# Kernel tuning notes

Measured on AMD Instinct MI355X. Metric: run time of the kernel, lower is better.

Reference implementation:

```python
import jax, jax.numpy as jnp
import numpy as np

N = 100000
E = 1600000
D = 128      # input_dim == hidden_dim
C = 40       # output_dim
L = 3        # num_layers
EPS = 1e-12  # F.normalize eps


def setup_inputs() -> dict:
    key = jax.random.key(0)
    ks = jax.random.split(key, 8)
    x = jax.random.normal(ks[0], (N, D), dtype=jnp.float32)
    edge_index = jax.random.randint(ks[1], (2, E), 0, N, dtype=jnp.int64)
    s = 1.0 / np.sqrt(D)
    # SAGEConv: lin_l (neighbor path, with bias), lin_r (root path, no bias)
    Wl = jax.random.uniform(ks[2], (L, D, D), jnp.float32, -s, s)
    bl = jax.random.uniform(ks[3], (L, D), jnp.float32, -s, s)
    Wr = jax.random.uniform(ks[4], (L, D, D), jnp.float32, -s, s)
    Wlin = jax.random.uniform(ks[5], (C, D), jnp.float32, -s, s)
    blin = jax.random.uniform(ks[6], (C,), jnp.float32, -s, s)
    return {"x": x, "edge_index": edge_index, "Wl": Wl, "bl": bl,
            "Wr": Wr, "Wlin": Wlin, "blin": blin}


def reference(x, edge_index, Wl, bl, Wr, Wlin, blin):
    src, dst = edge_index[0], edge_index[1]
    # in-degree counts for mean aggregation (computed once, reused per layer)
    cnt = jax.ops.segment_sum(jnp.ones((E,), jnp.float32), dst, num_segments=N)
    inv_cnt = (1.0 / jnp.maximum(cnt, 1.0))[:, None]  # [N,1]
    z = x
    for i in range(L):
        msg = z[src]  # gather [E, D]
        agg = jax.ops.segment_sum(msg, dst, num_segments=N) * inv_cnt  # mean [N, D]
        out = agg @ Wl[i].T + bl[i] + z @ Wr[i].T
        # SAGEConv normalize=True: L2 normalize per node
        nrm = jnp.linalg.norm(out, axis=-1, keepdims=True)
        out = out / jnp.maximum(nrm, EPS)
        z = jax.nn.relu(out)  # dropout p=0 -> identity
    return z @ Wlin.T + blin  # [N, C]
```

## Files before the change

kernel.cpp:

```cpp
#include <hip/hip_runtime.h>


typedef __bf16 bf16x8 __attribute__((ext_vector_type(8)));
typedef float  f32x4  __attribute__((ext_vector_type(4)));

#define MFMA16(a, b, c) __builtin_amdgcn_mfma_f32_16x16x32_bf16((a), (b), (c), 0, 0, 0)

__device__ __forceinline__ unsigned rne_bf16(float f) {
  unsigned u = __float_as_uint(f);
  unsigned r = u + 0x7FFFu + ((u >> 16) & 1u);
  return r >> 16;
}

__device__ __forceinline__ float bf_lo(unsigned u) { return __uint_as_float(u << 16); }
__device__ __forceinline__ float bf_hi(unsigned u) { return __uint_as_float(u & 0xFFFF0000u); }


__global__ void gcur_init_k(int* __restrict__ gcur, int cap) {
  gcur[threadIdx.x] = threadIdx.x * cap;
}

__global__ __launch_bounds__(256) void bucketA_k(
    const int* __restrict__ src, const int* __restrict__ dst,
    int* __restrict__ gcur, unsigned* __restrict__ coarse, int E, int nc) {
  __shared__ int hist[128];
  __shared__ int sd[128];
  __shared__ int lpos[128];
  __shared__ int gbase[128];
  __shared__ unsigned stage[2048];
  __shared__ unsigned char sbuck[2048];

  const int tid = threadIdx.x;
  const int e0 = blockIdx.x * 2048;

  if (tid < 128) hist[tid] = 0;
  __syncthreads();

  int bv[8], pk[8];
#pragma unroll
  for (int j = 0; j < 8; ++j) {
    int e = e0 + j * 256 + tid;
    bv[j] = -1;
    if (e < E) {
      int s = src[e], d = dst[e];
      bv[j] = d >> 10;
      pk[j] = s | ((d & 1023) << 17);
      atomicAdd(&hist[bv[j]], 1);
    }
  }
  __syncthreads();

  if (tid < 128) sd[tid] = hist[tid];
  __syncthreads();
  for (int off = 1; off < 128; off <<= 1) {
    int t = 0;
    if (tid < 128 && tid >= off) t = sd[tid - off];
    __syncthreads();
    if (tid < 128) sd[tid] += t;
    __syncthreads();
  }
  if (tid < 128) {
    int excl = sd[tid] - hist[tid];
    lpos[tid] = excl;
    gbase[tid] = (tid < nc && hist[tid] > 0) ? atomicAdd(&gcur[tid], hist[tid]) : 0;
  }
  __syncthreads();

#pragma unroll
  for (int j = 0; j < 8; ++j) {
    if (bv[j] >= 0) {
      int slot = atomicAdd(&lpos[bv[j]], 1);
      stage[slot] = (unsigned)pk[j];
      sbuck[slot] = (unsigned char)bv[j];
    }
  }
  __syncthreads();

  const int total = sd[127];
  for (int i = tid; i < total; i += 256) {
    int b = sbuck[i];
    int excl = sd[b] - hist[b];
    coarse[gbase[b] + (i - excl)] = stage[i];
  }
}

__global__ void cscan_k(const int* __restrict__ gcur, int cap, int nc,
                        int* __restrict__ cbase) {
  __shared__ int sd[128];
  const int tid = threadIdx.x;
  int v = (tid < nc) ? (gcur[tid] - tid * cap) : 0;
  sd[tid] = v;
  __syncthreads();
  for (int off = 1; off < 128; off <<= 1) {
    int u = (tid >= off) ? sd[tid - off] : 0;
    __syncthreads();
    sd[tid] += u;
    __syncthreads();
  }
  cbase[tid] = sd[tid] - v;
  if (tid == 127) cbase[128] = sd[127];
}

__global__ __launch_bounds__(256) void bucketB_k(
    const int* __restrict__ cbase, const int* __restrict__ gcur,
    const unsigned* __restrict__ coarse, int cap,
    int* __restrict__ esrc, int* __restrict__ offsets,
    float* __restrict__ inv_cnt, int n) {
  __shared__ int hcnt[1024];
  __shared__ int cur[1024];
  __shared__ int sd[256];

  const int tid = threadIdx.x;
  const int b = blockIdx.x;
  const int base = b * 1024;
  const int nn = (n - base < 1024) ? (n - base) : 1024;
  const int wbeg = b * cap;
  const int wend = gcur[b];
  const int gdst = cbase[b];

  for (int j = tid; j < 1024; j += 256) hcnt[j] = 0;
  __syncthreads();
  for (int idx = wbeg + tid; idx < wend; idx += 256)
    atomicAdd(&hcnt[coarse[idx] >> 17], 1);
  __syncthreads();

  int b0 = hcnt[tid * 4], b1 = hcnt[tid * 4 + 1];
  int b2 = hcnt[tid * 4 + 2], b3 = hcnt[tid * 4 + 3];
  int tot = b0 + b1 + b2 + b3;
  sd[tid] = tot;
  __syncthreads();
  for (int off = 1; off < 256; off <<= 1) {
    int u = (tid >= off) ? sd[tid - off] : 0;
    __syncthreads();
    sd[tid] += u;
    __syncthreads();
  }
  int excl = gdst + sd[tid] - tot;
  cur[tid * 4]     = excl;
  cur[tid * 4 + 1] = excl + b0;
  cur[tid * 4 + 2] = excl + b0 + b1;
  cur[tid * 4 + 3] = excl + b0 + b1 + b2;
  __syncthreads();

  for (int j = tid; j < nn; j += 256) {
    offsets[base + j] = cur[j];
    int c = hcnt[j] > 1 ? hcnt[j] : 1;
    inv_cnt[base + j] = 1.0f / (float)c;
  }
  if (tid == 0 && base + nn >= n) offsets[n] = gdst + (wend - wbeg);
  __syncthreads();

  for (int idx = wbeg + tid; idx < wend; idx += 256) {
    unsigned p = coarse[idx];
    int pos = atomicAdd(&cur[p >> 17], 1);
    esrc[pos] = (int)(p & 0x1FFFFu);
  }
}

__global__ void to_bf16_k(const float4* __restrict__ in, uint2* __restrict__ out, int n4) {
  int i = blockIdx.x * 256 + threadIdx.x;
  if (i >= n4) return;
  float4 f = in[i];
  uint2 o;
  o.x = rne_bf16(f.x) | (rne_bf16(f.y) << 16);
  o.y = rne_bf16(f.z) | (rne_bf16(f.w) << 16);
  out[i] = o;
}

__global__ void wfrag_prep_k(const float* __restrict__ Wl, const float* __restrict__ Wr,
                             unsigned short* __restrict__ wfrag) {
  int id = blockIdx.x * 256 + threadIdx.x;
  if (id >= 3 * 2 * 8 * 8 * 64) return;
  int l = id & 63;
  int c = (id >> 6) & 7;
  int t = (id >> 9) & 7;
  int p = (id >> 12) & 1;
  int layer = id >> 13;
  int col = t * 16 + (l & 15);
  int kbase = c * 32 + (l >> 4) * 8;
  unsigned short* dst = wfrag + (size_t)layer * 65536 +
                        ((((size_t)p * 8 + t) * 8 + c) * 64 + l) * 8;
#pragma unroll
  for (int j = 0; j < 8; ++j) {
    int k = kbase + j;
    float w = (k < 128) ? Wl[layer * 16384 + col * 128 + k]
                        : Wr[layer * 16384 + col * 128 + (k - 128)];
    unsigned h = rne_bf16(w);
    unsigned o;
    if (p == 0) o = h;
    else o = rne_bf16(w - __uint_as_float(h << 16));
    dst[j] = (unsigned short)o;
  }
}

__global__ void wlin_frag_k(const float* __restrict__ Wlin, unsigned short* __restrict__ wlf) {
  int id = blockIdx.x * 256 + threadIdx.x;
  if (id >= 3 * 4 * 64) return;
  int l = id & 63;
  int c = (id >> 6) & 3;
  int t = id >> 8;
  int col = t * 16 + (l & 15);
  int kbase = c * 32 + (l >> 4) * 8;
  unsigned short* dst = wlf + (size_t)id * 8;
#pragma unroll
  for (int j = 0; j < 8; ++j) {
    float w = (col < 40) ? Wlin[col * 128 + kbase + j] : 0.f;
    dst[j] = (unsigned short)rne_bf16(w);
  }
}

__global__ void aggregate_k(const unsigned short* __restrict__ zb,
                            const int* __restrict__ offsets,
                            const int* __restrict__ esrc,
                            const float* __restrict__ inv_cnt,
                            unsigned short* __restrict__ aggh, int n) {
  int node = (blockIdx.x * 256 + threadIdx.x) >> 4;
  int l16 = threadIdx.x & 15;
  if (node >= n) return;
  int beg = offsets[node], end = offsets[node + 1];
  float a0 = 0.f, a1 = 0.f, a2 = 0.f, a3 = 0.f;
  float a4 = 0.f, a5 = 0.f, a6 = 0.f, a7 = 0.f;
  int t = beg;
  for (; t + 4 <= end; t += 4) {
    int s0 = esrc[t], s1 = esrc[t + 1], s2 = esrc[t + 2], s3 = esrc[t + 3];
    uint4 d0 = *(const uint4*)(zb + (size_t)s0 * 128 + l16 * 8);
    uint4 d1 = *(const uint4*)(zb + (size_t)s1 * 128 + l16 * 8);
    uint4 d2 = *(const uint4*)(zb + (size_t)s2 * 128 + l16 * 8);
    uint4 d3 = *(const uint4*)(zb + (size_t)s3 * 128 + l16 * 8);
    a0 += bf_lo(d0.x); a1 += bf_hi(d0.x); a2 += bf_lo(d0.y); a3 += bf_hi(d0.y);
    a4 += bf_lo(d0.z); a5 += bf_hi(d0.z); a6 += bf_lo(d0.w); a7 += bf_hi(d0.w);
    a0 += bf_lo(d1.x); a1 += bf_hi(d1.x); a2 += bf_lo(d1.y); a3 += bf_hi(d1.y);
    a4 += bf_lo(d1.z); a5 += bf_hi(d1.z); a6 += bf_lo(d1.w); a7 += bf_hi(d1.w);
    a0 += bf_lo(d2.x); a1 += bf_hi(d2.x); a2 += bf_lo(d2.y); a3 += bf_hi(d2.y);
    a4 += bf_lo(d2.z); a5 += bf_hi(d2.z); a6 += bf_lo(d2.w); a7 += bf_hi(d2.w);
    a0 += bf_lo(d3.x); a1 += bf_hi(d3.x); a2 += bf_lo(d3.y); a3 += bf_hi(d3.y);
    a4 += bf_lo(d3.z); a5 += bf_hi(d3.z); a6 += bf_lo(d3.w); a7 += bf_hi(d3.w);
  }
  for (; t + 2 <= end; t += 2) {
    int s0 = esrc[t], s1 = esrc[t + 1];
    uint4 d0 = *(const uint4*)(zb + (size_t)s0 * 128 + l16 * 8);
    uint4 d1 = *(const uint4*)(zb + (size_t)s1 * 128 + l16 * 8);
    a0 += bf_lo(d0.x); a1 += bf_hi(d0.x); a2 += bf_lo(d0.y); a3 += bf_hi(d0.y);
    a4 += bf_lo(d0.z); a5 += bf_hi(d0.z); a6 += bf_lo(d0.w); a7 += bf_hi(d0.w);
    a0 += bf_lo(d1.x); a1 += bf_hi(d1.x); a2 += bf_lo(d1.y); a3 += bf_hi(d1.y);
    a4 += bf_lo(d1.z); a5 += bf_hi(d1.z); a6 += bf_lo(d1.w); a7 += bf_hi(d1.w);
  }
  if (t < end) {
    int s0 = esrc[t];
    uint4 d0 = *(const uint4*)(zb + (size_t)s0 * 128 + l16 * 8);
    a0 += bf_lo(d0.x); a1 += bf_hi(d0.x); a2 += bf_lo(d0.y); a3 += bf_hi(d0.y);
    a4 += bf_lo(d0.z); a5 += bf_hi(d0.z); a6 += bf_lo(d0.w); a7 += bf_hi(d0.w);
  }
  float ic = inv_cnt[node];
  uint4 hv;
  hv.x = rne_bf16(a0 * ic) | (rne_bf16(a1 * ic) << 16);
  hv.y = rne_bf16(a2 * ic) | (rne_bf16(a3 * ic) << 16);
  hv.z = rne_bf16(a4 * ic) | (rne_bf16(a5 * ic) << 16);
  hv.w = rne_bf16(a6 * ic) | (rne_bf16(a7 * ic) << 16);
  *(uint4*)(aggh + (size_t)node * 128 + l16 * 8) = hv;
}

__global__ __launch_bounds__(256) void sage_layer_mfma_k(
    const unsigned short* __restrict__ zb, const unsigned short* __restrict__ aggh,
    const unsigned short* __restrict__ wf, const float* __restrict__ bl,
    unsigned short* __restrict__ out_bf, int n, int ntiles) {
  __shared__ unsigned short Ah_s[32 * 256];
  __shared__ float psum[2][4][16];

  const int lane = threadIdx.x & 63;
  const int wv = threadIdx.x >> 6;
  const int g = lane >> 4;
  const int rl = lane & 15;

  const bf16x8* wfv = (const bf16x8*)wf;
  const int t0 = wv * 2, t1 = wv * 2 + 1;
  bf16x8 Bh0[8], Bh1[8], Bl0[8], Bl1[8];
#pragma unroll
  for (int c = 0; c < 8; ++c) {
    Bh0[c] = wfv[((0 * 8 + t0) * 8 + c) * 64 + lane];
    Bh1[c] = wfv[((0 * 8 + t1) * 8 + c) * 64 + lane];
    Bl0[c] = wfv[((1 * 8 + t0) * 8 + c) * 64 + lane];
    Bl1[c] = wfv[((1 * 8 + t1) * 8 + c) * 64 + lane];
  }
  const float b0 = bl[t0 * 16 + rl];
  const float b1 = bl[t1 * 16 + rl];

  char* pAh = (char*)Ah_s;

  for (int tile = blockIdx.x; tile < ntiles; tile += gridDim.x) {
    const int v0 = tile * 32;

#pragma unroll
    for (int q = 0; q < 2; ++q) {
      int lin = q * 2048 + threadIdx.x * 8;
      int r = lin >> 7;
      int col = lin & 127;
      int v = v0 + r; v = (v < n) ? v : (n - 1);
      int swz = (r & 7) << 4;
      uint4 dh = *(const uint4*)(aggh + (size_t)v * 128 + col);
      uint4 dz = *(const uint4*)(zb + (size_t)v * 128 + col);
      *(uint4*)(pAh + ((r * 512 + col * 2) ^ swz)) = dh;
      *(uint4*)(pAh + ((r * 512 + 256 + col * 2) ^ swz)) = dz;
    }
    __syncthreads();

#pragma unroll
    for (int s = 0; s < 2; ++s) {
      f32x4 a0 = {0.f, 0.f, 0.f, 0.f};
      f32x4 a1 = {0.f, 0.f, 0.f, 0.f};
      const int rowH = (s * 16 + rl) * 512;
      const int swz = (rl & 7) << 4;
#pragma unroll
      for (int c = 0; c < 8; ++c) {
        int offH = (rowH + c * 64 + g * 16) ^ swz;
        bf16x8 ah = *(const bf16x8*)(pAh + offH);
        a0 = MFMA16(ah, Bh0[c], a0); a1 = MFMA16(ah, Bh1[c], a1);
        a0 = MFMA16(ah, Bl0[c], a0); a1 = MFMA16(ah, Bl1[c], a1);
      }
      float pr[4];
#pragma unroll
      for (int j = 0; j < 4; ++j) {
        a0[j] += b0; a1[j] += b1;
        pr[j] = a0[j] * a0[j] + a1[j] * a1[j];
      }
#pragma unroll
      for (int m = 1; m < 16; m <<= 1) {
#pragma unroll
        for (int j = 0; j < 4; ++j) pr[j] += __shfl_xor(pr[j], m);
      }
      if (rl == 0) {
#pragma unroll
        for (int j = 0; j < 4; ++j) psum[s][wv][g * 4 + j] = pr[j];
      }
      __syncthreads();
#pragma unroll
      for (int j = 0; j < 4; ++j) {
        int row16 = g * 4 + j;
        float tot = psum[s][0][row16] + psum[s][1][row16] +
                    psum[s][2][row16] + psum[s][3][row16];
        float inv = 1.0f / fmaxf(sqrtf(tot), 1e-12f);
        int v = v0 + s * 16 + row16;
        if (v < n) {
          float o0 = fmaxf(a0[j] * inv, 0.f);
          float o1 = fmaxf(a1[j] * inv, 0.f);
          out_bf[(size_t)v * 128 + t0 * 16 + rl] = (unsigned short)rne_bf16(o0);
          out_bf[(size_t)v * 128 + t1 * 16 + rl] = (unsigned short)rne_bf16(o1);
        }
      }
    }
    __syncthreads();
  }
}

__global__ __launch_bounds__(256, 4) void final_linear_mfma_k(
    const unsigned short* __restrict__ zb, const unsigned short* __restrict__ wlf,
    const float* __restrict__ blin, float* __restrict__ out, int n, int ntiles) {
  __shared__ unsigned short Az[64 * 128];

  const int lane = threadIdx.x & 63;
  const int wv = threadIdx.x >> 6;
  const int g = lane >> 4;
  const int rl = lane & 15;

  const bf16x8* wv8 = (const bf16x8*)wlf;
  bf16x8 B[3][4];
#pragma unroll
  for (int t = 0; t < 3; ++t)
#pragma unroll
    for (int c = 0; c < 4; ++c) B[t][c] = wv8[(t * 4 + c) * 64 + lane];
  float bias[3];
#pragma unroll
  for (int t = 0; t < 3; ++t) {
    int col = t * 16 + rl;
    bias[t] = (col < 40) ? blin[col] : 0.f;
  }

  char* pAz = (char*)Az;

  for (int tile = blockIdx.x; tile < ntiles; tile += gridDim.x) {
    const int v0 = tile * 64;
#pragma unroll
    for (int q = 0; q < 4; ++q) {
      int lin = q * 2048 + threadIdx.x * 8;
      int r = lin >> 7;
      int col = lin & 127;
      int v = v0 + r; v = (v < n) ? v : (n - 1);
      uint4 d = *(const uint4*)(zb + (size_t)v * 128 + col);
      int byte = (r * 256 + col * 2) ^ ((r & 7) << 4);
      *(uint4*)(pAz + byte) = d;
    }
    __syncthreads();

    f32x4 acc0 = {0.f, 0.f, 0.f, 0.f};
    f32x4 acc1 = {0.f, 0.f, 0.f, 0.f};
    f32x4 acc2 = {0.f, 0.f, 0.f, 0.f};
    const int rowB = (wv * 16 + rl) * 256;
    const int swz = (rl & 7) << 4;
#pragma unroll
    for (int c = 0; c < 4; ++c) {
      int off = (rowB + c * 64 + g * 16) ^ swz;
      bf16x8 a = *(const bf16x8*)(pAz + off);
      acc0 = MFMA16(a, B[0][c], acc0);
      acc1 = MFMA16(a, B[1][c], acc1);
      acc2 = MFMA16(a, B[2][c], acc2);
    }
#pragma unroll
    for (int j = 0; j < 4; ++j) {
      int v = v0 + wv * 16 + g * 4 + j;
      if (v < n) {
        float* op = out + (size_t)v * 40;
        op[rl] = acc0[j] + bias[0];
        op[16 + rl] = acc1[j] + bias[1];
        if (rl < 8) op[32 + rl] = acc2[j] + bias[2];
      }
    }
    __syncthreads();
  }
}


extern "C" void kernel_launch(void* const* d_in, const int* in_sizes, int n_in,
                              void* d_out, int out_size, void* d_ws, size_t ws_size,
                              hipStream_t stream) {
  const float* x    = (const float*)d_in[0];
  const int*   ei   = (const int*)d_in[1];
  const float* Wl   = (const float*)d_in[2];
  const float* bl   = (const float*)d_in[3];
  const float* Wr   = (const float*)d_in[4];
  const float* Wlin = (const float*)d_in[5];
  const float* blin = (const float*)d_in[6];

  const int N = in_sizes[0] / 128;
  const int E = in_sizes[1] / 2;
  const int D = 128;
  const int NC = (N + 1023) >> 10;
  const int cap = (E + NC - 1) / NC + 4096;

  const int* src = ei;
  const int* dstp = ei + E;

  unsigned short* planeA = (unsigned short*)d_ws;
  unsigned short* planeB = planeA + (size_t)N * D;
  unsigned short* aggh   = planeB + (size_t)N * D;
  float* inv_cnt = (float*)(aggh + (size_t)N * D);
  unsigned short* wlf = (unsigned short*)(inv_cnt + N);
  unsigned short* Wfrag = wlf + 6144;
  int*   offsets = (int*)(Wfrag + 3 * 65536);
  int*   esrc    = offsets + N + 1;
  unsigned* coarse = (unsigned*)(esrc + E);
  int*   cbase   = (int*)(coarse + (size_t)NC * cap);
  int*   gcur    = cbase + 129;

  gcur_init_k<<<1, 128, 0, stream>>>(gcur, cap);
  bucketA_k<<<(E + 2047) / 2048, 256, 0, stream>>>(src, dstp, gcur, coarse, E, NC);
  cscan_k<<<1, 128, 0, stream>>>(gcur, cap, NC, cbase);
  bucketB_k<<<NC, 256, 0, stream>>>(cbase, gcur, coarse, cap, esrc, offsets, inv_cnt, N);

  wfrag_prep_k<<<96, 256, 0, stream>>>(Wl, Wr, Wfrag);
  wlin_frag_k<<<3, 256, 0, stream>>>(Wlin, wlf);
  to_bf16_k<<<((N * 32) + 255) / 256, 256, 0, stream>>>((const float4*)x, (uint2*)planeA, N * 32);

  const int aggGrid = (N * 16 + 255) / 256;
  const int ntiles = (N + 31) / 32;

  aggregate_k<<<aggGrid, 256, 0, stream>>>(planeA, offsets, esrc, inv_cnt, aggh, N);
  sage_layer_mfma_k<<<ntiles, 256, 0, stream>>>(planeA, aggh, Wfrag + 0 * 65536, bl + 0 * D, planeB, N, ntiles);
  aggregate_k<<<aggGrid, 256, 0, stream>>>(planeB, offsets, esrc, inv_cnt, aggh, N);
  sage_layer_mfma_k<<<ntiles, 256, 0, stream>>>(planeB, aggh, Wfrag + 1 * 65536, bl + 1 * D, planeA, N, ntiles);
  aggregate_k<<<aggGrid, 256, 0, stream>>>(planeA, offsets, esrc, inv_cnt, aggh, N);
  sage_layer_mfma_k<<<ntiles, 256, 0, stream>>>(planeA, aggh, Wfrag + 2 * 65536, bl + 2 * D, planeB, N, ntiles);

  const int ntiles64 = (N + 63) / 64;
  final_linear_mfma_k<<<ntiles64, 256, 0, stream>>>(planeB, wlf, blin, (float*)d_out, N, ntiles64);
}
```

Before: 376.4 us.

## Merge prep kernels, fold coarse scan into bucketB, fuse final linear into last layer

Merges the gcur init, weight-fragment prep, Wlin prep and x-to-bf16 conversion into one launch. The per-bucket prefix scan moves into each bucketB block, so every block redoes the small scan and the cscan kernel goes away. The last SAGE layer keeps its normalized bf16 activations in shared memory and applies the final 128x40 linear with MFMA directly, removing the write and reread of the last activation plane and one launch. The cost is extra shared memory and work in the last layer kernel, which may lower its occupancy.

```diff
diff --git a/kernel.cpp b/kernel.cpp
--- a/kernel.cpp
+++ b/kernel.cpp
@@ -15,10 +15,67 @@
 __device__ __forceinline__ float bf_lo(unsigned u) { return __uint_as_float(u << 16); }
 __device__ __forceinline__ float bf_hi(unsigned u) { return __uint_as_float(u & 0xFFFF0000u); }
 
-
-__global__ void gcur_init_k(int* __restrict__ gcur, int cap) {
-  gcur[threadIdx.x] = threadIdx.x * cap;
-}
+__global__ __launch_bounds__(256) void prep_k(
+    const float* __restrict__ x, const float* __restrict__ Wl,
+    const float* __restrict__ Wr, const float* __restrict__ Wlin,
+    uint2* __restrict__ planeA, unsigned short* __restrict__ wfrag,
+    unsigned short* __restrict__ wlf, int* __restrict__ gcur,
+    int cap, int n4) {
+  const int b = blockIdx.x;
+  const int tid = threadIdx.x;
+  if (b == 0) {
+    if (tid < 128) gcur[tid] = tid * cap;
+    return;
+  }
+  if (b <= 96) {
+    int id = (b - 1) * 256 + tid;
+    int l = id & 63;
+    int c = (id >> 6) & 7;
+    int t = (id >> 9) & 7;
+    int p = (id >> 12) & 1;
+    int layer = id >> 13;
+    int col = t * 16 + (l & 15);
+    int kbase = c * 32 + (l >> 4) * 8;
+    unsigned short* dst = wfrag + (size_t)layer * 65536 +
+                          ((((size_t)p * 8 + t) * 8 + c) * 64 + l) * 8;
+#pragma unroll
+    for (int j = 0; j < 8; ++j) {
+      int k = kbase + j;
+      float w = (k < 128) ? Wl[layer * 16384 + col * 128 + k]
+                          : Wr[layer * 16384 + col * 128 + (k - 128)];
+      unsigned h = rne_bf16(w);
+      unsigned o;
+      if (p == 0) o = h;
+      else o = rne_bf16(w - __uint_as_float(h << 16));
+      dst[j] = (unsigned short)o;
+    }
+    return;
+  }
+  if (b == 97) {
+    for (int id = tid; id < 3 * 4 * 64; id += 256) {
+      int l = id & 63;
+      int c = (id >> 6) & 3;
+      int t = id >> 8;
+      int col = t * 16 + (l & 15);
+      int kbase = c * 32 + (l >> 4) * 8;
+      unsigned short* dst = wlf + (size_t)id * 8;
+#pragma unroll
+      for (int j = 0; j < 8; ++j) {
+        float w = (col < 40) ? Wlin[col * 128 + kbase + j] : 0.f;
+        dst[j] = (unsigned short)rne_bf16(w);
+      }
+    }
+    return;
+  }
+  int i = (b - 98) * 256 + tid;
+  if (i >= n4) return;
+  float4 f = ((const float4*)x)[i];
+  uint2 o;
+  o.x = rne_bf16(f.x) | (rne_bf16(f.y) << 16);
+  o.y = rne_bf16(f.z) | (rne_bf16(f.w) << 16);
+  planeA[i] = o;
+}
+
 
 __global__ __launch_bounds__(256) void bucketA_k(
     const int* __restrict__ src, const int* __restrict__ dst,
@@ -84,31 +141,14 @@
   }
 }
 
-__global__ void cscan_k(const int* __restrict__ gcur, int cap, int nc,
-                        int* __restrict__ cbase) {
-  __shared__ int sd[128];
-  const int tid = threadIdx.x;
-  int v = (tid < nc) ? (gcur[tid] - tid * cap) : 0;
-  sd[tid] = v;
-  __syncthreads();
-  for (int off = 1; off < 128; off <<= 1) {
-    int u = (tid >= off) ? sd[tid - off] : 0;
-    __syncthreads();
-    sd[tid] += u;
-    __syncthreads();
-  }
-  cbase[tid] = sd[tid] - v;
-  if (tid == 127) cbase[128] = sd[127];
-}
-
 __global__ __launch_bounds__(256) void bucketB_k(
-    const int* __restrict__ cbase, const int* __restrict__ gcur,
-    const unsigned* __restrict__ coarse, int cap,
+    const int* __restrict__ gcur, const unsigned* __restrict__ coarse, int cap,
     int* __restrict__ esrc, int* __restrict__ offsets,
-    float* __restrict__ inv_cnt, int n) {
+    float* __restrict__ inv_cnt, int n, int nc) {
   __shared__ int hcnt[1024];
   __shared__ int cur[1024];
   __shared__ int sd[256];
+  __shared__ int sh_gdst;
 
   const int tid = threadIdx.x;
   const int b = blockIdx.x;
@@ -116,10 +156,24 @@
   const int nn = (n - base < 1024) ? (n - base) : 1024;
   const int wbeg = b * cap;
   const int wend = gcur[b];
-  const int gdst = cbase[b];
-
+
+  if (tid < 128) {
+    int v = (tid < nc) ? (gcur[tid] - tid * cap) : 0;
+    sd[tid] = v;
+  }
+  __syncthreads();
+  for (int off = 1; off < 128; off <<= 1) {
+    int u = 0;
+    if (tid < 128 && tid >= off) u = sd[tid - off];
+    __syncthreads();
+    if (tid < 128) sd[tid] += u;
+    __syncthreads();
+  }
+  if (tid == b) sh_gdst = sd[tid] - (wend - wbeg);
   for (int j = tid; j < 1024; j += 256) hcnt[j] = 0;
   __syncthreads();
+  const int gdst = sh_gdst;
+
   for (int idx = wbeg + tid; idx < wend; idx += 256)
     atomicAdd(&hcnt[coarse[idx] >> 17], 1);
   __syncthreads();
@@ -154,58 +208,6 @@
     unsigned p = coarse[idx];
     int pos = atomicAdd(&cur[p >> 17], 1);
     esrc[pos] = (int)(p & 0x1FFFFu);
-  }
-}
-
-__global__ void to_bf16_k(const float4* __restrict__ in, uint2* __restrict__ out, int n4) {
-  int i = blockIdx.x * 256 + threadIdx.x;
-  if (i >= n4) return;
-  float4 f = in[i];
-  uint2 o;
-  o.x = rne_bf16(f.x) | (rne_bf16(f.y) << 16);
-  o.y = rne_bf16(f.z) | (rne_bf16(f.w) << 16);
-  out[i] = o;
-}
-
-__global__ void wfrag_prep_k(const float* __restrict__ Wl, const float* __restrict__ Wr,
-                             unsigned short* __restrict__ wfrag) {
-  int id = blockIdx.x * 256 + threadIdx.x;
-  if (id >= 3 * 2 * 8 * 8 * 64) return;
-  int l = id & 63;
-  int c = (id >> 6) & 7;
-  int t = (id >> 9) & 7;
-  int p = (id >> 12) & 1;
-  int layer = id >> 13;
-  int col = t * 16 + (l & 15);
-  int kbase = c * 32 + (l >> 4) * 8;
-  unsigned short* dst = wfrag + (size_t)layer * 65536 +
-                        ((((size_t)p * 8 + t) * 8 + c) * 64 + l) * 8;
-#pragma unroll
-  for (int j = 0; j < 8; ++j) {
-    int k = kbase + j;
-    float w = (k < 128) ? Wl[layer * 16384 + col * 128 + k]
-                        : Wr[layer * 16384 + col * 128 + (k - 128)];
-    unsigned h = rne_bf16(w);
-    unsigned o;
-    if (p == 0) o = h;
-    else o = rne_bf16(w - __uint_as_float(h << 16));
-    dst[j] = (unsigned short)o;
-  }
-}
-
-__global__ void wlin_frag_k(const float* __restrict__ Wlin, unsigned short* __restrict__ wlf) {
-  int id = blockIdx.x * 256 + threadIdx.x;
-  if (id >= 3 * 4 * 64) return;
-  int l = id & 63;
-  int c = (id >> 6) & 3;
-  int t = id >> 8;
-  int col = t * 16 + (l & 15);
-  int kbase = c * 32 + (l >> 4) * 8;
-  unsigned short* dst = wlf + (size_t)id * 8;
-#pragma unroll
-  for (int j = 0; j < 8; ++j) {
-    float w = (col < 40) ? Wlin[col * 128 + kbase + j] : 0.f;
-    dst[j] = (unsigned short)rne_bf16(w);
   }
 }
 
@@ -260,11 +262,15 @@
   *(uint4*)(aggh + (size_t)node * 128 + l16 * 8) = hv;
 }
 
+template <bool FUSE>
 __global__ __launch_bounds__(256) void sage_layer_mfma_k(
     const unsigned short* __restrict__ zb, const unsigned short* __restrict__ aggh,
     const unsigned short* __restrict__ wf, const float* __restrict__ bl,
-    unsigned short* __restrict__ out_bf, int n, int ntiles) {
+    unsigned short* __restrict__ out_bf,
+    const unsigned short* __restrict__ wlf, const float* __restrict__ blin,
+    float* __restrict__ fout, int n, int ntiles) {
   __shared__ unsigned short Ah_s[32 * 256];
+  __shared__ unsigned short Zt_s[32 * 128];
   __shared__ float psum[2][4][16];
 
   const int lane = threadIdx.x & 63;
@@ -286,6 +292,8 @@
   const float b1 = bl[t1 * 16 + rl];
 
   char* pAh = (char*)Ah_s;
+  char* pZt = (char*)Zt_s;
+  const bf16x8* wlfv = (const bf16x8*)wlf;
 
   for (int tile = blockIdx.x; tile < ntiles; tile += gridDim.x) {
     const int v0 = tile * 32;
@@ -340,78 +348,46 @@
                     psum[s][2][row16] + psum[s][3][row16];
         float inv = 1.0f / fmaxf(sqrtf(tot), 1e-12f);
         int v = v0 + s * 16 + row16;
-        if (v < n) {
-          float o0 = fmaxf(a0[j] * inv, 0.f);
-          float o1 = fmaxf(a1[j] * inv, 0.f);
-          out_bf[(size_t)v * 128 + t0 * 16 + rl] = (unsigned short)rne_bf16(o0);
-          out_bf[(size_t)v * 128 + t1 * 16 + rl] = (unsigned short)rne_bf16(o1);
+        float o0 = fmaxf(a0[j] * inv, 0.f);
+        float o1 = fmaxf(a1[j] * inv, 0.f);
+        unsigned short q0 = (unsigned short)rne_bf16(o0);
+        unsigned short q1 = (unsigned short)rne_bf16(o1);
+        if (!FUSE) {
+          if (v < n) {
+            out_bf[(size_t)v * 128 + t0 * 16 + rl] = q0;
+            out_bf[(size_t)v * 128 + t1 * 16 + rl] = q1;
+          }
+        } else {
+          int rloc = s * 16 + row16;
+          int sw = (rloc & 7) << 4;
+          *(unsigned short*)(pZt + ((rloc * 256 + (t0 * 16 + rl) * 2) ^ sw)) = q0;
+          *(unsigned short*)(pZt + ((rloc * 256 + (t1 * 16 + rl) * 2) ^ sw)) = q1;
         }
       }
     }
-    __syncthreads();
-  }
-}
-
-__global__ __launch_bounds__(256, 4) void final_linear_mfma_k(
-    const unsigned short* __restrict__ zb, const unsigned short* __restrict__ wlf,
-    const float* __restrict__ blin, float* __restrict__ out, int n, int ntiles) {
-  __shared__ unsigned short Az[64 * 128];
-
-  const int lane = threadIdx.x & 63;
-  const int wv = threadIdx.x >> 6;
-  const int g = lane >> 4;
-  const int rl = lane & 15;
-
-  const bf16x8* wv8 = (const bf16x8*)wlf;
-  bf16x8 B[3][4];
-#pragma unroll
-  for (int t = 0; t < 3; ++t)
-#pragma unroll
-    for (int c = 0; c < 4; ++c) B[t][c] = wv8[(t * 4 + c) * 64 + lane];
-  float bias[3];
-#pragma unroll
-  for (int t = 0; t < 3; ++t) {
-    int col = t * 16 + rl;
-    bias[t] = (col < 40) ? blin[col] : 0.f;
-  }
-
-  char* pAz = (char*)Az;
-
-  for (int tile = blockIdx.x; tile < ntiles; tile += gridDim.x) {
-    const int v0 = tile * 64;
-#pragma unroll
-    for (int q = 0; q < 4; ++q) {
-      int lin = q * 2048 + threadIdx.x * 8;
-      int r = lin >> 7;
-      int col = lin & 127;
-      int v = v0 + r; v = (v < n) ? v : (n - 1);
-      uint4 d = *(const uint4*)(zb + (size_t)v * 128 + col);
-      int byte = (r * 256 + col * 2) ^ ((r & 7) << 4);
-      *(uint4*)(pAz + byte) = d;
-    }
-    __syncthreads();
-
-    f32x4 acc0 = {0.f, 0.f, 0.f, 0.f};
-    f32x4 acc1 = {0.f, 0.f, 0.f, 0.f};
-    f32x4 acc2 = {0.f, 0.f, 0.f, 0.f};
-    const int rowB = (wv * 16 + rl) * 256;
-    const int swz = (rl & 7) << 4;
-#pragma unroll
-    for (int c = 0; c < 4; ++c) {
-      int off = (rowB + c * 64 + g * 16) ^ swz;
-      bf16x8 a = *(const bf16x8*)(pAz + off);
-      acc0 = MFMA16(a, B[0][c], acc0);
-      acc1 = MFMA16(a, B[1][c], acc1);
-      acc2 = MFMA16(a, B[2][c], acc2);
-    }
-#pragma unroll
-    for (int j = 0; j < 4; ++j) {
-      int v = v0 + wv * 16 + g * 4 + j;
-      if (v < n) {
-        float* op = out + (size_t)v * 40;
-        op[rl] = acc0[j] + bias[0];
-        op[16 + rl] = acc1[j] + bias[1];
-        if (rl < 8) op[32 + rl] = acc2[j] + bias[2];
+
+    if (FUSE) {
+      __syncthreads();
+      for (int job = wv; job < 6; job += 4) {
+        int s = job / 3, t = job % 3;
+        f32x4 acc = {0.f, 0.f, 0.f, 0.f};
+        const int rowz = s * 16 + rl;
+        const int swzz = (rowz & 7) << 4;
+#pragma unroll
+        for (int c = 0; c < 4; ++c) {
+          bf16x8 a = *(const bf16x8*)(pZt + ((rowz * 256 + c * 64 + g * 16) ^ swzz));
+          bf16x8 bw = wlfv[(t * 4 + c) * 64 + lane];
+          acc = MFMA16(a, bw, acc);
+        }
+        int col = t * 16 + rl;
+        if (col < 40) {
+          float bb = blin[col];
+#pragma unroll
+          for (int j = 0; j < 4; ++j) {
+            int v = v0 + s * 16 + g * 4 + j;
+            if (v < n) fout[(size_t)v * 40 + col] = acc[j] + bb;
+          }
+        }
       }
     }
     __syncthreads();
@@ -448,28 +424,26 @@
   int*   offsets = (int*)(Wfrag + 3 * 65536);
   int*   esrc    = offsets + N + 1;
   unsigned* coarse = (unsigned*)(esrc + E);
-  int*   cbase   = (int*)(coarse + (size_t)NC * cap);
-  int*   gcur    = cbase + 129;
-
-  gcur_init_k<<<1, 128, 0, stream>>>(gcur, cap);
+  int*   gcur    = (int*)(coarse + (size_t)NC * cap);
+
+  const int n4 = N * 32;
+  prep_k<<<98 + (n4 + 255) / 256, 256, 0, stream>>>(
+      x, Wl, Wr, Wlin, (uint2*)planeA, Wfrag, wlf, gcur, cap, n4);
+
   bucketA_k<<<(E + 2047) / 2048, 256, 0, stream>>>(src, dstp, gcur, coarse, E, NC);
-  cscan_k<<<1, 128, 0, stream>>>(gcur, cap, NC, cbase);
-  bucketB_k<<<NC, 256, 0, stream>>>(cbase, gcur, coarse, cap, esrc, offsets, inv_cnt, N);
-
-  wfrag_prep_k<<<96, 256, 0, stream>>>(Wl, Wr, Wfrag);
-  wlin_frag_k<<<3, 256, 0, stream>>>(Wlin, wlf);
-  to_bf16_k<<<((N * 32) + 255) / 256, 256, 0, stream>>>((const float4*)x, (uint2*)planeA, N * 32);
+  bucketB_k<<<NC, 256, 0, stream>>>(gcur, coarse, cap, esrc, offsets, inv_cnt, N, NC);
 
   const int aggGrid = (N * 16 + 255) / 256;
   const int ntiles = (N + 31) / 32;
 
   aggregate_k<<<aggGrid, 256, 0, stream>>>(planeA, offsets, esrc, inv_cnt, aggh, N);
-  sage_layer_mfma_k<<<ntiles, 256, 0, stream>>>(planeA, aggh, Wfrag + 0 * 65536, bl + 0 * D, planeB, N, ntiles);
+  sage_layer_mfma_k<false><<<ntiles, 256, 0, stream>>>(
+      planeA, aggh, Wfrag + 0 * 65536, bl + 0 * D, planeB, wlf, blin, nullptr, N, ntiles);
   aggregate_k<<<aggGrid, 256, 0, stream>>>(planeB, offsets, esrc, inv_cnt, aggh, N);
-  sage_layer_mfma_k<<<ntiles, 256, 0, stream>>>(planeB, aggh, Wfrag + 1 * 65536, bl + 1 * D, planeA, N, ntiles);
+  sage_layer_mfma_k<false><<<ntiles, 256, 0, stream>>>(
+      planeB, aggh, Wfrag + 1 * 65536, bl + 1 * D, planeA, wlf, blin, nullptr, N, ntiles);
   aggregate_k<<<aggGrid, 256, 0, stream>>>(planeA, offsets, esrc, inv_cnt, aggh, N);
-  sage_layer_mfma_k<<<ntiles, 256, 0, stream>>>(planeA, aggh, Wfrag + 2 * 65536, bl + 2 * D, planeB, N, ntiles);
-
-  const int ntiles64 = (N + 63) / 64;
-  final_linear_mfma_k<<<ntiles64, 256, 0, stream>>>(planeB, wlf, blin, (float*)d_out, N, ntiles64);
-}
+  sage_layer_mfma_k<true><<<ntiles, 256, 0, stream>>>(
+      planeA, aggh, Wfrag + 2 * 65536, bl + 2 * D, nullptr, wlf, blin,
+      (float*)d_out, N, ntiles);
+}
```

After: 366.8 us. 2.6% less time.
